# Kernel optimization log

Measured on AMD Instinct MI355X. Metric: run time of the kernel, lower is better.

Reference implementation:

```python
import jax, jax.numpy as jnp
import numpy as np

SIZE = 1024      # codebook size
DIM = 64         # latent_dim
TOPK = 3
BETA_C = 0.25
LEGACY = False

def setup_inputs() -> dict:
    key = jax.random.key(0)
    kz, ke = jax.random.split(key)
    z = jax.random.normal(kz, (16, 64, 64, DIM), dtype=jnp.float32)
    # nn.Embedding init: uniform(-1/size, 1/size)
    emb = jax.random.uniform(ke, (SIZE, DIM), minval=-1.0 / SIZE, maxval=1.0 / SIZE, dtype=jnp.float32)
    return {"z": z, "emb": emb}

def reference(z, emb):
    zf = z.reshape(-1, DIM)                                  # [N, D]
    # squared euclidean distances via matmul expansion: [N, SIZE]
    d = (jnp.sum(zf ** 2, axis=1, keepdims=True)
         + jnp.sum(emb ** 2, axis=1)
         - 2.0 * (zf @ emb.T))
    neg_d, topk_idx = jax.lax.top_k(-d, TOPK)                # smallest distances -> [N, K]
    # direct gather instead of one-hot matmul (same math)
    z_q = jnp.mean(emb[topk_idx], axis=1).reshape(z.shape)   # [N,K,D] -> [N,D] -> z.shape
    if LEGACY:
        loss = (jnp.mean((jax.lax.stop_gradient(z_q) - z) ** 2)
                + BETA_C * jnp.mean((z_q - jax.lax.stop_gradient(z)) ** 2))
    else:
        loss = (BETA_C * jnp.mean((jax.lax.stop_gradient(z_q) - z) ** 2)
                + jnp.mean((z_q - jax.lax.stop_gradient(z)) ** 2))
    # one-hot encodings are part of the module's return signature
    topk_encodings = jax.nn.one_hot(topk_idx, SIZE, dtype=z.dtype)   # [N, K, SIZE]
    e_mean = jnp.mean(topk_encodings, axis=(0, 1))                   # [SIZE]
    perplexity = jnp.exp(-jnp.sum(e_mean * jnp.log(e_mean + 1e-10)))
    z_q_st = z + jax.lax.stop_gradient(z_q - z)              # straight-through estimator
    return (z_q_st, loss, perplexity, topk_encodings, topk_idx)
```

## Files before the change

### kernel.cpp

```cpp
#include <hip/hip_runtime.h>
#include <math.h>

#define N_ROWS 65536
#define CB 1024
#define SPLITS 4
#define JS (CB / SPLITS)

__device__ __forceinline__ float tree_sum64_sq(const float* x) {
#pragma clang fp contract(off)
    float sq[64];
#pragma unroll
    for (int i = 0; i < 64; ++i) sq[i] = x[i] * x[i];
    float s[16];
#pragma unroll
    for (int l = 0; l < 16; ++l) s[l] = (sq[l] + sq[l + 16]) + (sq[l + 32] + sq[l + 48]);
    float t[8];
#pragma unroll
    for (int l = 0; l < 8; ++l) t[l] = s[l] + s[l + 8];
    float u[4];
#pragma unroll
    for (int l = 0; l < 4; ++l) u[l] = t[l] + t[l + 4];
    float v0 = u[0] + u[2];
    float v1 = u[1] + u[3];
    return v0 + v1;
}

__device__ __forceinline__ void top3_insert(float d, int j,
                                            float& v0, float& v1, float& v2,
                                            int& i0, int& i1, int& i2) {
    bool b0 = d < v0, b1 = d < v1, b2 = d < v2;
    v2 = b1 ? v1 : (b2 ? d : v2);
    i2 = b1 ? i1 : (b2 ? j : i2);
    v1 = b0 ? v0 : (b1 ? d : v1);
    i1 = b0 ? i0 : (b1 ? j : i1);
    v0 = b0 ? d : v0;
    i0 = b0 ? j : i0;
}

__global__ __launch_bounds__(256) void embB_kernel(const float* __restrict__ emb,
                                                   float* __restrict__ B) {
    int j = blockIdx.x * 256 + threadIdx.x;
    if (j >= CB) return;
    float e[64];
    const float4* e4 = (const float4*)(emb + (size_t)j * 64);
#pragma unroll
    for (int k = 0; k < 16; ++k) {
        float4 v = e4[k];
        e[4 * k] = v.x; e[4 * k + 1] = v.y; e[4 * k + 2] = v.z; e[4 * k + 3] = v.w;
    }
    B[j] = tree_sum64_sq(e);
}

__global__ __launch_bounds__(256) void score_fused_kernel(const float* __restrict__ z,
                                                          const float* __restrict__ emb,
                                                          const float* __restrict__ B,
                                                          float* __restrict__ out3,
                                                          float* __restrict__ scrD,
                                                          int* __restrict__ scrI) {
    const int bid = blockIdx.x;
    const int split = bid & (SPLITS - 1);
    const int rowBlk = bid >> 2;
    const int t = threadIdx.x;
    const int row = rowBlk * 256 + t;

    float zr[64];
    const float4* z4 = (const float4*)(z + (size_t)row * 64);
#pragma unroll
    for (int k = 0; k < 16; ++k) {
        float4 v = z4[k];
        zr[4 * k] = v.x; zr[4 * k + 1] = v.y; zr[4 * k + 2] = v.z; zr[4 * k + 3] = v.w;
    }
    float A = tree_sum64_sq(zr);

    float4* zb = (float4*)out3 + (size_t)rowBlk * 196608 + (size_t)split * 49152;
    const float4 zero4 = make_float4(0.0f, 0.0f, 0.0f, 0.0f);

    float v0 = 3.402823466e38f, v1 = 3.402823466e38f, v2 = 3.402823466e38f;
    int i0 = 0, i1 = 0, i2 = 0;
    const int jbase = split * JS;

    for (int g = 0; g < 64; ++g) {
        zb[(size_t)(3 * g + 0) * 256 + t] = zero4;
        zb[(size_t)(3 * g + 1) * 256 + t] = zero4;
        zb[(size_t)(3 * g + 2) * 256 + t] = zero4;

#pragma unroll
        for (int u = 0; u < 4; u += 2) {
            const int j0 = jbase + 4 * g + u;
            const int j1 = j0 + 1;
            const float4* e0p = (const float4*)(emb + (size_t)j0 * 64);
            const float4* e1p = (const float4*)(emb + (size_t)j1 * 64);
            float b0v = B[j0], b1v = B[j1];
            float a0 = 0.0f, a1 = 0.0f;
#pragma unroll
            for (int k = 0; k < 16; ++k) {
                float4 e0 = e0p[k], e1 = e1p[k];
                float x0 = zr[4 * k], x1 = zr[4 * k + 1];
                float x2 = zr[4 * k + 2], x3 = zr[4 * k + 3];
                a0 = fmaf(x0, e0.x, a0); a0 = fmaf(x1, e0.y, a0);
                a0 = fmaf(x2, e0.z, a0); a0 = fmaf(x3, e0.w, a0);
                a1 = fmaf(x0, e1.x, a1); a1 = fmaf(x1, e1.y, a1);
                a1 = fmaf(x2, e1.z, a1); a1 = fmaf(x3, e1.w, a1);
            }
            float d0 = (A + b0v) - 2.0f * a0;
            float d1 = (A + b1v) - 2.0f * a1;
            top3_insert(d0, j0, v0, v1, v2, i0, i1, i2);
            top3_insert(d1, j1, v0, v1, v2, i0, i1, i2);
        }
    }

    size_t o = ((size_t)split * N_ROWS + row) * 3;
    scrD[o] = v0; scrD[o + 1] = v1; scrD[o + 2] = v2;
    scrI[o] = i0; scrI[o + 1] = i1; scrI[o + 2] = i2;
}

__global__ __launch_bounds__(256) void merge_kernel(const float* __restrict__ z,
                                                    const float* __restrict__ emb,
                                                    const float* __restrict__ scrD,
                                                    const int* __restrict__ scrI,
                                                    float* __restrict__ out0,
                                                    float* __restrict__ out3,
                                                    float* __restrict__ out4,
                                                    int* __restrict__ hist,
                                                    float* __restrict__ lossAcc) {
    int row = blockIdx.x * 256 + threadIdx.x;

    float v0 = 3.402823466e38f, v1 = 3.402823466e38f, v2 = 3.402823466e38f;
    int i0 = 0, i1 = 0, i2 = 0;
#pragma unroll
    for (int s = 0; s < SPLITS; ++s) {
        size_t o = ((size_t)s * N_ROWS + row) * 3;
#pragma unroll
        for (int t = 0; t < 3; ++t) {
            float d = scrD[o + t];
            int j = scrI[o + t];
            top3_insert(d, j, v0, v1, v2, i0, i1, i2);
        }
    }

    size_t rb = (size_t)row * 3072;
    out3[rb + i0]        = 1.0f;
    out3[rb + 1024 + i1] = 1.0f;
    out3[rb + 2048 + i2] = 1.0f;

    const float* e0 = emb + (size_t)i0 * 64;
    const float* e1 = emb + (size_t)i1 * 64;
    const float* e2 = emb + (size_t)i2 * 64;
    const float4* z4 = (const float4*)(z + (size_t)row * 64);
    float4* o4 = (float4*)(out0 + (size_t)row * 64);

    float lsum = 0.0f;
#pragma unroll
    for (int k4 = 0; k4 < 16; ++k4) {
        float4 zv = z4[k4];
        float4 st;
        {
            int k = 4 * k4;
            float zq = ((e0[k] + e1[k]) + e2[k]) / 3.0f;
            float df = zq - zv.x;
            st.x = zv.x + df;
            lsum = fmaf(df, df, lsum);
        }
        {
            int k = 4 * k4 + 1;
            float zq = ((e0[k] + e1[k]) + e2[k]) / 3.0f;
            float df = zq - zv.y;
            st.y = zv.y + df;
            lsum = fmaf(df, df, lsum);
        }
        {
            int k = 4 * k4 + 2;
            float zq = ((e0[k] + e1[k]) + e2[k]) / 3.0f;
            float df = zq - zv.z;
            st.z = zv.z + df;
            lsum = fmaf(df, df, lsum);
        }
        {
            int k = 4 * k4 + 3;
            float zq = ((e0[k] + e1[k]) + e2[k]) / 3.0f;
            float df = zq - zv.w;
            st.w = zv.w + df;
            lsum = fmaf(df, df, lsum);
        }
        o4[k4] = st;
    }

    size_t ob = (size_t)row * 3;
    out4[ob]     = (float)i0;
    out4[ob + 1] = (float)i1;
    out4[ob + 2] = (float)i2;
    atomicAdd(&hist[i0], 1);
    atomicAdd(&hist[i1], 1);
    atomicAdd(&hist[i2], 1);

#pragma unroll
    for (int off = 32; off >= 1; off >>= 1) lsum += __shfl_down(lsum, off);
    if ((threadIdx.x & 63) == 0) atomicAdd(lossAcc, lsum);
}

__global__ __launch_bounds__(256) void finalize_kernel(const int* __restrict__ hist,
                                                       const float* __restrict__ lossAcc,
                                                       float* __restrict__ out1,
                                                       float* __restrict__ out2) {
    __shared__ float red[256];
    int t = threadIdx.x;
    float local = 0.0f;
    for (int b = t; b < CB; b += 256) {
        float em = (float)hist[b] / 196608.0f;
        local += em * logf(em + 1e-10f);
    }
    red[t] = local;
    __syncthreads();
    for (int s = 128; s >= 1; s >>= 1) {
        if (t < s) red[t] += red[t + s];
        __syncthreads();
    }
    if (t == 0) {
        *out2 = expf(-red[0]);
        float m = *lossAcc / 4194304.0f;
        *out1 = 0.25f * m + m;
    }
}

extern "C" void kernel_launch(void* const* d_in, const int* in_sizes, int n_in,
                              void* d_out, int out_size, void* d_ws, size_t ws_size,
                              hipStream_t stream) {
    const float* z   = (const float*)d_in[0];
    const float* emb = (const float*)d_in[1];

    float* out  = (float*)d_out;
    float* out0 = out;
    float* out1 = out + 4194304;
    float* out2 = out + 4194305;
    float* out3 = out + 4194306;
    float* out4 = out + 4194306 + 201326592ll;

    int*   hist    = (int*)d_ws;
    float* lossAcc = (float*)((char*)d_ws + 4096);
    float* B       = (float*)((char*)d_ws + 8192);
    float* scrD = (float*)((char*)d_ws + 16384);
    int*   scrI = (int*)((char*)d_ws + 16384 + (size_t)SPLITS * N_ROWS * 3 * 4);

    hipMemsetAsync(d_ws, 0, 4096 + 16, stream);

    embB_kernel<<<4, 256, 0, stream>>>(emb, B);
    score_fused_kernel<<<(N_ROWS / 256) * SPLITS, 256, 0, stream>>>(z, emb, B,
                                                                    out3, scrD, scrI);
    merge_kernel<<<N_ROWS / 256, 256, 0, stream>>>(z, emb, scrD, scrI,
                                                   out0, out3, out4, hist, lossAcc);
    finalize_kernel<<<1, 256, 0, stream>>>(hist, lossAcc, out1, out2);
}
```

Before: 1.182 ms.

## Move one-hot writes to merge kernel and fold codebook norms into score kernel

The zero-fill of the 800MB one-hot output moves out of the score kernel. The merge kernel now writes each one-hot row fully, including the ones, with coalesced float4 stores, so the old pass of zero stores plus scattered single ones is gone. Codebook squared norms are now computed per block into shared memory, and hist and loss are zeroed inside the score kernel, which removes the embB kernel and the memset launch. Risks: the score kernel becomes lighter while the merge kernel carries the whole output write with fewer blocks. Zeroing hist inside block 0 relies on the kernels running in stream order.

Result: slower. 1.377 ms (+16.5%).

```diff
diff --git a/kernel.cpp b/kernel.cpp
--- a/kernel.cpp
+++ b/kernel.cpp
@@ -37,31 +37,36 @@
     i0 = b0 ? j : i0;
 }
 
-__global__ __launch_bounds__(256) void embB_kernel(const float* __restrict__ emb,
-                                                   float* __restrict__ B) {
-    int j = blockIdx.x * 256 + threadIdx.x;
-    if (j >= CB) return;
-    float e[64];
-    const float4* e4 = (const float4*)(emb + (size_t)j * 64);
-#pragma unroll
-    for (int k = 0; k < 16; ++k) {
-        float4 v = e4[k];
-        e[4 * k] = v.x; e[4 * k + 1] = v.y; e[4 * k + 2] = v.z; e[4 * k + 3] = v.w;
-    }
-    B[j] = tree_sum64_sq(e);
-}
-
-__global__ __launch_bounds__(256) void score_fused_kernel(const float* __restrict__ z,
-                                                          const float* __restrict__ emb,
-                                                          const float* __restrict__ B,
-                                                          float* __restrict__ out3,
-                                                          float* __restrict__ scrD,
-                                                          int* __restrict__ scrI) {
+__global__ __launch_bounds__(256, 4) void score_kernel(const float* __restrict__ z,
+                                                       const float* __restrict__ emb,
+                                                       float* __restrict__ scrD,
+                                                       int* __restrict__ scrI,
+                                                       int* __restrict__ hist,
+                                                       float* __restrict__ lossAcc) {
     const int bid = blockIdx.x;
     const int split = bid & (SPLITS - 1);
     const int rowBlk = bid >> 2;
     const int t = threadIdx.x;
     const int row = rowBlk * 256 + t;
+    const int jbase = split * JS;
+
+    if (bid == 0) {
+        hist[t] = 0; hist[t + 256] = 0; hist[t + 512] = 0; hist[t + 768] = 0;
+        if (t == 0) *lossAcc = 0.0f;
+    }
+
+    __shared__ float Bsh[JS];
+    {
+        float e[64];
+        const float4* e4 = (const float4*)(emb + (size_t)(jbase + t) * 64);
+#pragma unroll
+        for (int k = 0; k < 16; ++k) {
+            float4 v = e4[k];
+            e[4 * k] = v.x; e[4 * k + 1] = v.y; e[4 * k + 2] = v.z; e[4 * k + 3] = v.w;
+        }
+        Bsh[t] = tree_sum64_sq(e);
+    }
+    __syncthreads();
 
     float zr[64];
     const float4* z4 = (const float4*)(z + (size_t)row * 64);
@@ -72,25 +77,18 @@
     }
     float A = tree_sum64_sq(zr);
 
-    float4* zb = (float4*)out3 + (size_t)rowBlk * 196608 + (size_t)split * 49152;
-    const float4 zero4 = make_float4(0.0f, 0.0f, 0.0f, 0.0f);
-
     float v0 = 3.402823466e38f, v1 = 3.402823466e38f, v2 = 3.402823466e38f;
     int i0 = 0, i1 = 0, i2 = 0;
-    const int jbase = split * JS;
 
     for (int g = 0; g < 64; ++g) {
-        zb[(size_t)(3 * g + 0) * 256 + t] = zero4;
-        zb[(size_t)(3 * g + 1) * 256 + t] = zero4;
-        zb[(size_t)(3 * g + 2) * 256 + t] = zero4;
-
 #pragma unroll
         for (int u = 0; u < 4; u += 2) {
             const int j0 = jbase + 4 * g + u;
             const int j1 = j0 + 1;
             const float4* e0p = (const float4*)(emb + (size_t)j0 * 64);
             const float4* e1p = (const float4*)(emb + (size_t)j1 * 64);
-            float b0v = B[j0], b1v = B[j1];
+            float b0v = Bsh[4 * g + u];
+            float b1v = Bsh[4 * g + u + 1];
             float a0 = 0.0f, a1 = 0.0f;
 #pragma unroll
             for (int k = 0; k < 16; ++k) {
@@ -114,16 +112,17 @@
     scrI[o] = i0; scrI[o + 1] = i1; scrI[o + 2] = i2;
 }
 
-__global__ __launch_bounds__(256) void merge_kernel(const float* __restrict__ z,
-                                                    const float* __restrict__ emb,
-                                                    const float* __restrict__ scrD,
-                                                    const int* __restrict__ scrI,
-                                                    float* __restrict__ out0,
-                                                    float* __restrict__ out3,
-                                                    float* __restrict__ out4,
-                                                    int* __restrict__ hist,
-                                                    float* __restrict__ lossAcc) {
-    int row = blockIdx.x * 256 + threadIdx.x;
+__global__ __launch_bounds__(256) void merge_onehot_kernel(const float* __restrict__ z,
+                                                           const float* __restrict__ emb,
+                                                           const float* __restrict__ scrD,
+                                                           const int* __restrict__ scrI,
+                                                           float* __restrict__ out0,
+                                                           float* __restrict__ out3,
+                                                           float* __restrict__ out4,
+                                                           int* __restrict__ hist,
+                                                           float* __restrict__ lossAcc) {
+    const int t = threadIdx.x;
+    const int row = blockIdx.x * 256 + t;
 
     float v0 = 3.402823466e38f, v1 = 3.402823466e38f, v2 = 3.402823466e38f;
     int i0 = 0, i1 = 0, i2 = 0;
@@ -131,17 +130,17 @@
     for (int s = 0; s < SPLITS; ++s) {
         size_t o = ((size_t)s * N_ROWS + row) * 3;
 #pragma unroll
-        for (int t = 0; t < 3; ++t) {
-            float d = scrD[o + t];
-            int j = scrI[o + t];
+        for (int q = 0; q < 3; ++q) {
+            float d = scrD[o + q];
+            int j = scrI[o + q];
             top3_insert(d, j, v0, v1, v2, i0, i1, i2);
         }
     }
 
-    size_t rb = (size_t)row * 3072;
-    out3[rb + i0]        = 1.0f;
-    out3[rb + 1024 + i1] = 1.0f;
-    out3[rb + 2048 + i2] = 1.0f;
+    __shared__ int sidx[256 * 3];
+    sidx[3 * t]     = i0;
+    sidx[3 * t + 1] = i1;
+    sidx[3 * t + 2] = i2;
 
     const float* e0 = emb + (size_t)i0 * 64;
     const float* e1 = emb + (size_t)i1 * 64;
@@ -195,7 +194,28 @@
 
 #pragma unroll
     for (int off = 32; off >= 1; off >>= 1) lsum += __shfl_down(lsum, off);
-    if ((threadIdx.x & 63) == 0) atomicAdd(lossAcc, lsum);
+    if ((t & 63) == 0) atomicAdd(lossAcc, lsum);
+
+    __syncthreads();
+
+    float4* p = (float4*)(out3 + (size_t)blockIdx.x * 256 * 3072);
+    const int c = 4 * t;
+    for (int r = 0; r < 256; ++r) {
+        int j0 = sidx[3 * r];
+        int j1 = sidx[3 * r + 1];
+        int j2 = sidx[3 * r + 2];
+        float4 w0, w1, w2;
+        w0.x = (c == j0) ? 1.0f : 0.0f; w0.y = (c + 1 == j0) ? 1.0f : 0.0f;
+        w0.z = (c + 2 == j0) ? 1.0f : 0.0f; w0.w = (c + 3 == j0) ? 1.0f : 0.0f;
+        w1.x = (c == j1) ? 1.0f : 0.0f; w1.y = (c + 1 == j1) ? 1.0f : 0.0f;
+        w1.z = (c + 2 == j1) ? 1.0f : 0.0f; w1.w = (c + 3 == j1) ? 1.0f : 0.0f;
+        w2.x = (c == j2) ? 1.0f : 0.0f; w2.y = (c + 1 == j2) ? 1.0f : 0.0f;
+        w2.z = (c + 2 == j2) ? 1.0f : 0.0f; w2.w = (c + 3 == j2) ? 1.0f : 0.0f;
+        size_t rbase = (size_t)r * 768;
+        p[rbase + t]       = w0;
+        p[rbase + 256 + t] = w1;
+        p[rbase + 512 + t] = w2;
+    }
 }
 
 __global__ __launch_bounds__(256) void finalize_kernel(const int* __restrict__ hist,
@@ -237,16 +257,13 @@
 
     int*   hist    = (int*)d_ws;
     float* lossAcc = (float*)((char*)d_ws + 4096);
-    float* B       = (float*)((char*)d_ws + 8192);
-    float* scrD = (float*)((char*)d_ws + 16384);
-    int*   scrI = (int*)((char*)d_ws + 16384 + (size_t)SPLITS * N_ROWS * 3 * 4);
-
-    hipMemsetAsync(d_ws, 0, 4096 + 16, stream);
-
-    embB_kernel<<<4, 256, 0, stream>>>(emb, B);
-    score_fused_kernel<<<(N_ROWS / 256) * SPLITS, 256, 0, stream>>>(z, emb, B,
-                                                                    out3, scrD, scrI);
-    merge_kernel<<<N_ROWS / 256, 256, 0, stream>>>(z, emb, scrD, scrI,
-                                                   out0, out3, out4, hist, lossAcc);
+    float* scrD    = (float*)((char*)d_ws + 16384);
+    int*   scrI    = (int*)((char*)d_ws + 16384 + (size_t)SPLITS * N_ROWS * 3 * 4);
+
+    score_kernel<<<(N_ROWS / 256) * SPLITS, 256, 0, stream>>>(z, emb, scrD, scrI,
+                                                              hist, lossAcc);
+    merge_onehot_kernel<<<N_ROWS / 256, 256, 0, stream>>>(z, emb, scrD, scrI,
+                                                          out0, out3, out4,
+                                                          hist, lossAcc);
     finalize_kernel<<<1, 256, 0, stream>>>(hist, lossAcc, out1, out2);
 }
```
